# Kernel optimization log

Hardware: AMD Instinct MI355X
Metric: run time of the kernel (lower is better)

## Reference

```python
import jax, jax.numpy as jnp
import numpy as np

WS = 7           # window size
NH = 12          # num heads
EPS_ADA = 1e-6   # AdaLayerNorm eps
EPS_LN = 1e-5    # torch nn.LayerNorm default eps


def _rel_pos_index(ws):
    coords = np.stack(np.meshgrid(np.arange(ws), np.arange(ws), indexing='ij'))  # (2,ws,ws)
    flat = coords.reshape(2, -1)                      # (2, N)
    rel = flat[:, :, None] - flat[:, None, :]         # (2, N, N)
    rel = rel.transpose(1, 2, 0).astype(np.int64)     # (N, N, 2)
    rel[:, :, 0] += ws - 1
    rel[:, :, 1] += ws - 1
    rel[:, :, 0] *= 2 * ws - 1
    return jnp.asarray(rel.sum(-1))                   # (N, N) in [0, (2ws-1)^2)

REL_IDX = _rel_pos_index(WS)


def setup_inputs() -> dict:
    key = jax.random.key(0)
    ks = jax.random.split(key, 8)
    B, H, W, C, COND = 32, 56, 56, 384, 128
    L = H * W
    s = 0.02
    return {
        'x_tok': jax.random.normal(ks[0], (B, L, C), jnp.float32),
        'z_tok': jax.random.normal(ks[1], (B, L, C), jnp.float32),
        'cond': jax.random.normal(ks[2], (B, COND), jnp.float32),
        'gamma_x': jnp.ones((C,), jnp.float32),
        'beta_x': jnp.zeros((C,), jnp.float32),
        'mod_w': jax.random.normal(ks[3], (COND, 2 * C), jnp.float32) * s,
        'mod_b': jnp.zeros((2 * C,), jnp.float32),
        'gamma_z': jnp.ones((C,), jnp.float32),
        'beta_z': jnp.zeros((C,), jnp.float32),
        'rel_bias_table': jax.random.normal(ks[4], ((2 * WS - 1) ** 2, NH), jnp.float32) * s,
        'q_w': jax.random.normal(ks[5], (C, C), jnp.float32) * s,
        'q_b': jnp.zeros((C,), jnp.float32),
        'kv_w': jax.random.normal(ks[6], (C, 2 * C), jnp.float32) * s,
        'kv_b': jnp.zeros((2 * C,), jnp.float32),
        'proj_w': jax.random.normal(ks[7], (C, C), jnp.float32) * s,
        'proj_b': jnp.zeros((C,), jnp.float32),
        'H': H,
        'W': W,
    }


def reference(x_tok, z_tok, cond, gamma_x, beta_x, mod_w, mod_b,
              gamma_z, beta_z, rel_bias_table, q_w, q_b, kv_w, kv_b,
              proj_w, proj_b, H, W):
    B, L, C = x_tok.shape
    hd = C // NH
    N = WS * WS

    # AdaLayerNorm-Zero on x
    mu = x_tok.mean(-1, keepdims=True)
    var = ((x_tok - mu) ** 2).mean(-1, keepdims=True)
    x_hat = (x_tok - mu) * jax.lax.rsqrt(var + EPS_ADA)
    mod = (cond @ mod_w + mod_b).reshape(B, 2, C)
    d_gamma, d_beta = mod[:, 0], mod[:, 1]
    x = (gamma_x * (1.0 + d_gamma))[:, None, :] * x_hat + (beta_x + d_beta)[:, None, :]

    # LayerNorm on z
    mz = z_tok.mean(-1, keepdims=True)
    vz = ((z_tok - mz) ** 2).mean(-1, keepdims=True)
    z = (z_tok - mz) * jax.lax.rsqrt(vz + EPS_LN) * gamma_z + beta_z

    # window partition: (B,H,W,C) -> (B*nW, N, C)
    def part(t):
        t = t.reshape(B, H // WS, WS, W // WS, WS, C)
        return t.transpose(0, 1, 3, 2, 4, 5).reshape(-1, N, C)

    x_win = part(x.reshape(B, H, W, C))
    z_win = part(z.reshape(B, H, W, C))

    # cross window attention
    q = (x_win @ q_w + q_b).reshape(-1, N, NH, hd).transpose(0, 2, 1, 3)  # (Bw,H,N,d)
    kv = (z_win @ kv_w + kv_b).reshape(-1, N, 2, NH, hd)
    k = kv[:, :, 0].transpose(0, 2, 1, 3)
    v = kv[:, :, 1].transpose(0, 2, 1, 3)
    scale = hd ** -0.5
    attn = jnp.einsum('bhnd,bhmd->bhnm', q * scale, k)                    # (Bw,H,N,N)
    bias = rel_bias_table[REL_IDX.reshape(-1)].reshape(N, N, NH).transpose(2, 0, 1)
    attn = jax.nn.softmax(attn + bias[None], axis=-1)
    out = jnp.einsum('bhnm,bhmd->bhnd', attn, v).transpose(0, 2, 1, 3).reshape(-1, N, C)
    out = out @ proj_w + proj_b

    # window reverse: (B*nW, N, C) -> (B, L, C)
    fused = out.reshape(B, H // WS, W // WS, WS, WS, C)
    fused = fused.transpose(0, 1, 3, 2, 4, 5).reshape(B, L, C)

    return x_tok + fused
```

## Files before the change

### kernel.cpp

```cpp
#include <hip/hip_runtime.h>
#include <hip/hip_bf16.h>

typedef float f32x4 __attribute__((ext_vector_type(4)));
typedef short short8 __attribute__((ext_vector_type(8)));
typedef __hip_bfloat16 bf16;

constexpr int CDIM  = 384;
constexpr int LTOK  = 3136;
constexpr int NWIN  = 2048;
constexpr int MROWS = 100352;
constexpr int MPAD  = MROWS + 64;
constexpr int NP64  = 1568;

__device__ __forceinline__ void gload_lds16(const void* g, void* l) {
  __builtin_amdgcn_global_load_lds(
      (const __attribute__((address_space(1))) void*)g,
      (__attribute__((address_space(3))) void*)l, 16, 0, 0);
}

__device__ __forceinline__ void row_to_bl(int r, int& b, int& l) {
  int w = r / 49, n = r % 49;
  b = w >> 6;
  int wrem = w & 63;
  int wy = wrem >> 3, wx = wrem & 7;
  int ny = n / 7, nx = n % 7;
  l = (wy * 7 + ny) * 56 + wx * 7 + nx;
}


__global__ __launch_bounds__(256) void prep_all(
    const float* __restrict__ cond, const float* __restrict__ mw,
    const float* __restrict__ mb, float* __restrict__ mod,
    const float* __restrict__ qw, const float* __restrict__ kvw,
    const float* __restrict__ pw,
    bf16* __restrict__ wtq, bf16* __restrict__ wtkv, bf16* __restrict__ wtp,
    const float* __restrict__ tab, float* __restrict__ bT) {
  int bid = blockIdx.x, t = threadIdx.x;
  if (bid < 96) {
    int idx = bid * 256 + t;
    int b = idx / 768, j = idx % 768;
    float s = mb[j];
    const float* cr = cond + b * 128;
    #pragma unroll 4
    for (int k = 0; k < 128; k++) s += cr[k] * mw[(size_t)k * 768 + j];
    mod[idx] = s;
  } else if (bid < 2400) {
    int idx = (bid - 96) * 256 + t;
    const float* src; bf16* dst; int i, Wn;
    if (idx < 147456)      { i = idx;          src = qw;  dst = wtq;  Wn = 384; }
    else if (idx < 442368) { i = idx - 147456; src = kvw; dst = wtkv; Wn = 768; }
    else                   { i = idx - 442368; src = pw;  dst = wtp;  Wn = 384; }
    int j = i & 7, nc = (i >> 3) & 63, g = (i >> 9) & 3;
    int kt = (i >> 11) % 12, s = i / 24576;
    int k = kt * 32 + g * 8 + j, n = s * 64 + nc;
    dst[i] = __float2bfloat16(src[(size_t)k * Wn + n]);
  } else {
    int idx = (bid - 2400) * 256 + t;
    int h = idx >> 12, rem = idx & 4095, m = rem >> 6, c = rem & 63;
    float v;
    if (c >= 49)      v = -1e30f;
    else if (m >= 49) v = 0.f;
    else {
      int yq = m / 7, xq = m % 7, yk = c / 7, xk = c % 7;
      v = tab[((yq - yk + 6) * 13 + (xq - xk + 6)) * 12 + h];
    }
    bT[idx] = v;
  }
}


struct alignas(8) B4 { bf16 h[4]; };

__global__ __launch_bounds__(256) void ln_both(
    const float* __restrict__ x_tok, const float* __restrict__ gx,
    const float* __restrict__ bx, const float* __restrict__ modbuf,
    const float* __restrict__ z_tok, const float* __restrict__ gz,
    const float* __restrict__ bz,
    bf16* __restrict__ xO, bf16* __restrict__ zO) {
  int bid = blockIdx.x;
  bool isX = bid < 25088;
  const float* src   = isX ? x_tok : z_tok;
  const float* gamma = isX ? gx : gz;
  const float* beta  = isX ? bx : bz;
  const float* mod   = isX ? modbuf : nullptr;
  bf16* dst          = isX ? xO : zO;
  float eps          = isX ? 1e-6f : 1e-5f;
  int rb = (isX ? bid : bid - 25088) * 4;

  int wid = threadIdx.x >> 6, lane = threadIdx.x & 63;
  int r = rb + wid;
  int bb, ll; row_to_bl(r, bb, ll);
  const f32x4* x4 = (const f32x4*)(src + ((size_t)bb * LTOK + ll) * 384);
  f32x4 a = x4[lane];
  f32x4 b = {0.f, 0.f, 0.f, 0.f};
  if (lane < 32) b = x4[64 + lane];
  float s  = a[0] + a[1] + a[2] + a[3] + b[0] + b[1] + b[2] + b[3];
  float s2 = a[0]*a[0] + a[1]*a[1] + a[2]*a[2] + a[3]*a[3]
           + b[0]*b[0] + b[1]*b[1] + b[2]*b[2] + b[3]*b[3];
  #pragma unroll
  for (int d = 1; d < 64; d <<= 1) { s += __shfl_xor(s, d); s2 += __shfl_xor(s2, d); }
  float mu = s * (1.f / 384.f);
  float var = s2 * (1.f / 384.f) - mu * mu;
  float rstd = rsqrtf(var + eps);
  bf16* o = dst + (size_t)r * 384;
  const f32x4* g4 = (const f32x4*)gamma;
  const f32x4* be4 = (const f32x4*)beta;
  if (mod != nullptr) {
    const f32x4* mg4 = (const f32x4*)(mod + bb * 768);
    const f32x4* mb4 = (const f32x4*)(mod + bb * 768 + 384);
    {
      f32x4 gg = g4[lane], bb2 = be4[lane], mg = mg4[lane], mb = mb4[lane];
      B4 p;
      #pragma unroll
      for (int i = 0; i < 4; i++)
        p.h[i] = __float2bfloat16((gg[i] * (1.f + mg[i])) * ((a[i] - mu) * rstd) + bb2[i] + mb[i]);
      *((B4*)o + lane) = p;
    }
    if (lane < 32) {
      f32x4 gg = g4[64 + lane], bb2 = be4[64 + lane], mg = mg4[64 + lane], mb = mb4[64 + lane];
      B4 p;
      #pragma unroll
      for (int i = 0; i < 4; i++)
        p.h[i] = __float2bfloat16((gg[i] * (1.f + mg[i])) * ((b[i] - mu) * rstd) + bb2[i] + mb[i]);
      *((B4*)o + 64 + lane) = p;
    }
  } else {
    {
      f32x4 gg = g4[lane], bb2 = be4[lane];
      B4 p;
      #pragma unroll
      for (int i = 0; i < 4; i++)
        p.h[i] = __float2bfloat16((a[i] - mu) * rstd * gg[i] + bb2[i]);
      *((B4*)o + lane) = p;
    }
    if (lane < 32) {
      f32x4 gg = g4[64 + lane], bb2 = be4[64 + lane];
      B4 p;
      #pragma unroll
      for (int i = 0; i < 4; i++)
        p.h[i] = __float2bfloat16((b[i] - mu) * rstd * gg[i] + bb2[i]);
      *((B4*)o + 64 + lane) = p;
    }
  }
}


template<int MODE>
__global__ __launch_bounds__(256, 4) void gemm6(
    const bf16* __restrict__ A, const bf16* __restrict__ WTt,
    const float* __restrict__ bias, void* __restrict__ outp,
    const float* __restrict__ resid, float scale, int N, int NS, int BPS) {
  __shared__ __align__(16) bf16 wS[24576];
  const int t = threadIdx.x;
  const int wid = t >> 6, lane = t & 63;
  const int r16 = lane & 15, g = lane >> 4;
  const int s = blockIdx.x % NS, bi = blockIdx.x / NS;

  {
    const char* src = (const char*)WTt + (size_t)s * 49152;
    #pragma unroll
    for (int i = 0; i < 12; i++)
      gload_lds16(src + (i * 256 + t) * 16, (char*)wS + (i * 256 + t) * 16);
  }
  float bc[4];
  #pragma unroll
  for (int ni = 0; ni < 4; ni++) bc[ni] = bias[s * 64 + ni * 16 + r16];
  __syncthreads();

  for (int p = bi; p < NP64; p += BPS) {
    const int prow = p * 64 + wid * 16;

    short8 aF[12];
    #pragma unroll
    for (int kt = 0; kt < 12; kt++)
      aF[kt] = *(const short8*)(A + (size_t)(prow + r16) * 384 + kt * 32 + g * 8);

    f32x4 acc[4] = {};
    #pragma unroll
    for (int kt = 0; kt < 12; kt++) {
      #pragma unroll
      for (int ni = 0; ni < 4; ni++) {
        short8 wF = *(const short8*)((const char*)wS + (kt * 4 + g) * 1024 + (ni * 16 + r16) * 16);
        acc[ni] = __builtin_amdgcn_mfma_f32_16x16x32_bf16(aF[kt], wF, acc[ni], 0, 0, 0);
      }
    }

    if (MODE == 0) {
      bf16* O = (bf16*)outp;
      #pragma unroll
      for (int rr = 0; rr < 4; rr++) {
        size_t rbase = (size_t)(prow + g * 4 + rr) * N + s * 64;
        #pragma unroll
        for (int ni = 0; ni < 4; ni++)
          O[rbase + ni * 16 + r16] = __float2bfloat16((acc[ni][rr] + bc[ni]) * scale);
      }
    } else {
      float* O = (float*)outp;
      #pragma unroll
      for (int rr = 0; rr < 4; rr++) {
        int row = prow + g * 4 + rr;
        int bb, ll; row_to_bl(row, bb, ll);
        size_t base = ((size_t)bb * LTOK + ll) * 384 + s * 64;
        #pragma unroll
        for (int ni = 0; ni < 4; ni++)
          O[base + ni * 16 + r16] = resid[base + ni * 16 + r16] + acc[ni][rr] + bc[ni];
      }
    }
  }
}


__global__ __launch_bounds__(64) void attn_kernel(
    const bf16* __restrict__ q, const bf16* __restrict__ kv,
    const float* __restrict__ biasT, bf16* __restrict__ o) {
  __shared__ __align__(16) bf16 vt[32][72];
  __shared__ __align__(16) bf16 P[64][72];
  const int h = blockIdx.x, w = blockIdx.y;
  const int lane = threadIdx.x;
  const int r16 = lane & 15, g = lane >> 4;
  const size_t qbase = (size_t)w * 49 * 384 + h * 32;
  const size_t kvbase = (size_t)w * 49 * 768 + h * 32;

  for (int e = lane; e < 32 * 72; e += 64) ((bf16*)vt)[e] = __float2bfloat16(0.f);
  for (int e = lane; e < 49 * 32; e += 64) {
    int c = e >> 5, d = e & 31;
    vt[d][c] = kv[kvbase + (size_t)c * 768 + 384 + d];
  }

  short8 aq[4], bk[4];
  #pragma unroll
  for (int mi = 0; mi < 4; mi++)
    aq[mi] = *(const short8*)(q + qbase + (size_t)(mi * 16 + r16) * 384 + g * 8);
  #pragma unroll
  for (int ni = 0; ni < 4; ni++)
    bk[ni] = *(const short8*)(kv + kvbase + (size_t)(ni * 16 + r16) * 768 + g * 8);

  f32x4 zero = {0.f, 0.f, 0.f, 0.f};
  f32x4 S[4][4];
  #pragma unroll
  for (int mi = 0; mi < 4; mi++)
    #pragma unroll
    for (int ni = 0; ni < 4; ni++)
      S[mi][ni] = __builtin_amdgcn_mfma_f32_16x16x32_bf16(aq[mi], bk[ni], zero, 0, 0, 0);

  const float* bt = biasT + h * 4096;
  #pragma unroll
  for (int mi = 0; mi < 4; mi++) {
    #pragma unroll
    for (int r = 0; r < 4; r++) {
      int rowm = mi * 16 + g * 4 + r;
      float sv[4];
      #pragma unroll
      for (int ni = 0; ni < 4; ni++)
        sv[ni] = S[mi][ni][r] + bt[rowm * 64 + ni * 16 + r16];
      float mx = fmaxf(fmaxf(sv[0], sv[1]), fmaxf(sv[2], sv[3]));
      #pragma unroll
      for (int d = 1; d < 16; d <<= 1) mx = fmaxf(mx, __shfl_xor(mx, d));
      float sum = 0.f;
      #pragma unroll
      for (int ni = 0; ni < 4; ni++) { sv[ni] = __expf(sv[ni] - mx); sum += sv[ni]; }
      #pragma unroll
      for (int d = 1; d < 16; d <<= 1) sum += __shfl_xor(sum, d);
      float inv = __fdividef(1.f, sum);
      #pragma unroll
      for (int ni = 0; ni < 4; ni++)
        P[rowm][ni * 16 + r16] = __float2bfloat16(sv[ni] * inv);
    }
  }
  __syncthreads();

  f32x4 acc[4][2] = {};
  #pragma unroll
  for (int c0 = 0; c0 < 2; c0++) {
    short8 ap[4], bv[2];
    #pragma unroll
    for (int mi = 0; mi < 4; mi++)
      ap[mi] = *(const short8*)((const char*)&P[0][0] + (mi * 16 + r16) * 144 + c0 * 64 + g * 16);
    #pragma unroll
    for (int di = 0; di < 2; di++)
      bv[di] = *(const short8*)((const char*)&vt[0][0] + (di * 16 + r16) * 144 + c0 * 64 + g * 16);
    #pragma unroll
    for (int mi = 0; mi < 4; mi++)
      #pragma unroll
      for (int di = 0; di < 2; di++)
        acc[mi][di] = __builtin_amdgcn_mfma_f32_16x16x32_bf16(ap[mi], bv[di], acc[mi][di], 0, 0, 0);
  }

  #pragma unroll
  for (int mi = 0; mi < 4; mi++) {
    #pragma unroll
    for (int r = 0; r < 4; r++) {
      int m = mi * 16 + g * 4 + r;
      if (m < 49) {
        #pragma unroll
        for (int di = 0; di < 2; di++)
          o[(size_t)(w * 49 + m) * 384 + h * 32 + di * 16 + r16] =
              __float2bfloat16(acc[mi][di][r]);
      }
    }
  }
}


extern "C" void kernel_launch(void* const* d_in, const int* in_sizes, int n_in,
                              void* d_out, int out_size, void* d_ws, size_t ws_size,
                              hipStream_t stream) {
  (void)in_sizes; (void)n_in; (void)out_size; (void)ws_size;
  const float* x_tok   = (const float*)d_in[0];
  const float* z_tok   = (const float*)d_in[1];
  const float* cond    = (const float*)d_in[2];
  const float* gamma_x = (const float*)d_in[3];
  const float* beta_x  = (const float*)d_in[4];
  const float* mod_w   = (const float*)d_in[5];
  const float* mod_b   = (const float*)d_in[6];
  const float* gamma_z = (const float*)d_in[7];
  const float* beta_z  = (const float*)d_in[8];
  const float* rel_tab = (const float*)d_in[9];
  const float* q_w     = (const float*)d_in[10];
  const float* q_b     = (const float*)d_in[11];
  const float* kv_w    = (const float*)d_in[12];
  const float* kv_b    = (const float*)d_in[13];
  const float* proj_w  = (const float*)d_in[14];
  const float* proj_b  = (const float*)d_in[15];

  char* ws = (char*)d_ws;
  float* modbuf = (float*)(ws + 0);
  bf16*  wtq    = (bf16*)(ws + 98304);
  bf16*  wtkv   = (bf16*)(ws + 98304 + 294912);
  bf16*  wtp    = (bf16*)(ws + 98304 + 294912 + 589824);
  float* biasT  = (float*)(ws + 98304 + 294912 + 589824 + 294912);
  char*  R1     = ws + 1474560;
  char*  R2     = R1 + (size_t)MPAD * 384 * 2;
  char*  R3     = R2 + (size_t)MPAD * 384 * 2;
  char*  R4     = R3 + (size_t)MPAD * 768 * 2;

  hipMemsetAsync(R2 + (size_t)MROWS * 384 * 2, 0, 64 * 384 * 2, stream);
  hipMemsetAsync(R3 + (size_t)MROWS * 768 * 2, 0, 64 * 768 * 2, stream);

  prep_all<<<2592, 256, 0, stream>>>(cond, mod_w, mod_b, modbuf,
                                     q_w, kv_w, proj_w, wtq, wtkv, wtp,
                                     rel_tab, biasT);
  ln_both<<<50176, 256, 0, stream>>>(x_tok, gamma_x, beta_x, modbuf,
                                     z_tok, gamma_z, beta_z,
                                     (bf16*)R1, (bf16*)R4);
  gemm6<0><<<768, 256, 0, stream>>>(
      (const bf16*)R1, wtq, q_b, R2, nullptr, 0.17677669529663687f, 384, 6, 128);
  gemm6<0><<<768, 256, 0, stream>>>(
      (const bf16*)R4, wtkv, kv_b, R3, nullptr, 1.0f, 768, 12, 64);
  attn_kernel<<<dim3(12, NWIN), 64, 0, stream>>>(
      (const bf16*)R2, (const bf16*)R3, biasT, (bf16*)R1);
  gemm6<1><<<768, 256, 0, stream>>>(
      (const bf16*)R1, wtp, proj_b, d_out, x_tok, 1.0f, 384, 6, 128);
}
```

Baseline: 704.6 us.

## Retile projection GEMMs to 128x32 blocks with 2x2 MFMA per wave

Each GEMM block now keeps a 32-column weight slice in LDS instead of 64 columns, halving shared memory and raising the occupancy target to 6 blocks per CU. Each wave computes a 32x32 tile (2x2 MFMA) rather than 16x64, and A fragments are loaded per k-step instead of being prefetched into 12 registers. The weight pre-layout is changed to match, and the grid is doubled with an x-swizzle so that groups of 8 blocks share row chunks. The intent is higher occupancy and better L2 locality for the A operand. In exchange, each A row tile is now read by twice as many column-slice blocks.

Measured after the change: 1.177 ms. 67.0% more time.

```diff
diff --git a/kernel.cpp b/kernel.cpp
--- a/kernel.cpp
+++ b/kernel.cpp
@@ -10,7 +10,7 @@
 constexpr int NWIN  = 2048;
 constexpr int MROWS = 100352;
 constexpr int MPAD  = MROWS + 64;
-constexpr int NP64  = 1568;
+constexpr int NP128 = 784;
 
 __device__ __forceinline__ void gload_lds16(const void* g, void* l) {
   __builtin_amdgcn_global_load_lds(
@@ -50,9 +50,11 @@
     if (idx < 147456)      { i = idx;          src = qw;  dst = wtq;  Wn = 384; }
     else if (idx < 442368) { i = idx - 147456; src = kvw; dst = wtkv; Wn = 768; }
     else                   { i = idx - 442368; src = pw;  dst = wtp;  Wn = 384; }
-    int j = i & 7, nc = (i >> 3) & 63, g = (i >> 9) & 3;
-    int kt = (i >> 11) % 12, s = i / 24576;
-    int k = kt * 32 + g * 8 + j, n = s * 64 + nc;
+    int s = i / 12288, rem = i % 12288;
+    int u = rem >> 8, v = rem & 255;
+    int ni = v >> 7, r16 = (v >> 3) & 15, j8 = v & 7;
+    int kt = u >> 2, g = u & 3;
+    int k = kt * 32 + g * 8 + j8, n = s * 32 + ni * 16 + r16;
     dst[i] = __float2bfloat16(src[(size_t)k * Wn + n]);
   } else {
     int idx = (bid - 2400) * 256 + t;
@@ -146,64 +148,68 @@
 
 
 template<int MODE>
-__global__ __launch_bounds__(256, 4) void gemm6(
+__global__ __launch_bounds__(256, 6) void gemm7(
     const bf16* __restrict__ A, const bf16* __restrict__ WTt,
     const float* __restrict__ bias, void* __restrict__ outp,
-    const float* __restrict__ resid, float scale, int N, int NS, int BPS) {
-  __shared__ __align__(16) bf16 wS[24576];
+    const float* __restrict__ resid, float scale, int N, int NS, int NC) {
+  __shared__ __align__(16) bf16 wS[12288];
   const int t = threadIdx.x;
   const int wid = t >> 6, lane = t & 63;
   const int r16 = lane & 15, g = lane >> 4;
-  const int s = blockIdx.x % NS, bi = blockIdx.x / NS;
+  const int x = blockIdx.x & 7, i = blockIdx.x >> 3;
+  const int s = i % NS;
+  const int c = (i / NS) * 8 + x;
 
   {
-    const char* src = (const char*)WTt + (size_t)s * 49152;
-    #pragma unroll
-    for (int i = 0; i < 12; i++)
-      gload_lds16(src + (i * 256 + t) * 16, (char*)wS + (i * 256 + t) * 16);
-  }
-  float bc[4];
-  #pragma unroll
-  for (int ni = 0; ni < 4; ni++) bc[ni] = bias[s * 64 + ni * 16 + r16];
+    const char* src = (const char*)WTt + (size_t)s * 24576;
+    #pragma unroll
+    for (int k = 0; k < 6; k++)
+      gload_lds16(src + (k * 256 + t) * 16, (char*)wS + (k * 256 + t) * 16);
+  }
+  const float bc0 = bias[s * 32 + r16];
+  const float bc1 = bias[s * 32 + 16 + r16];
   __syncthreads();
 
-  for (int p = bi; p < NP64; p += BPS) {
-    const int prow = p * 64 + wid * 16;
-
-    short8 aF[12];
-    #pragma unroll
-    for (int kt = 0; kt < 12; kt++)
-      aF[kt] = *(const short8*)(A + (size_t)(prow + r16) * 384 + kt * 32 + g * 8);
-
-    f32x4 acc[4] = {};
+  for (int p = c; p < NP128; p += NC) {
+    const int prow = p * 128 + wid * 32;
+    const bf16* Ab = A + (size_t)prow * 384;
+
+    f32x4 acc[2][2] = {};
     #pragma unroll
     for (int kt = 0; kt < 12; kt++) {
-      #pragma unroll
-      for (int ni = 0; ni < 4; ni++) {
-        short8 wF = *(const short8*)((const char*)wS + (kt * 4 + g) * 1024 + (ni * 16 + r16) * 16);
-        acc[ni] = __builtin_amdgcn_mfma_f32_16x16x32_bf16(aF[kt], wF, acc[ni], 0, 0, 0);
-      }
+      short8 a0 = *(const short8*)(Ab + (size_t)r16 * 384 + kt * 32 + g * 8);
+      short8 a1 = *(const short8*)(Ab + (size_t)(16 + r16) * 384 + kt * 32 + g * 8);
+      short8 w0 = *(const short8*)((const char*)wS + (kt * 4 + g) * 512 + r16 * 16);
+      short8 w1 = *(const short8*)((const char*)wS + (kt * 4 + g) * 512 + 256 + r16 * 16);
+      acc[0][0] = __builtin_amdgcn_mfma_f32_16x16x32_bf16(a0, w0, acc[0][0], 0, 0, 0);
+      acc[0][1] = __builtin_amdgcn_mfma_f32_16x16x32_bf16(a0, w1, acc[0][1], 0, 0, 0);
+      acc[1][0] = __builtin_amdgcn_mfma_f32_16x16x32_bf16(a1, w0, acc[1][0], 0, 0, 0);
+      acc[1][1] = __builtin_amdgcn_mfma_f32_16x16x32_bf16(a1, w1, acc[1][1], 0, 0, 0);
     }
 
     if (MODE == 0) {
       bf16* O = (bf16*)outp;
       #pragma unroll
-      for (int rr = 0; rr < 4; rr++) {
-        size_t rbase = (size_t)(prow + g * 4 + rr) * N + s * 64;
+      for (int m = 0; m < 2; m++) {
         #pragma unroll
-        for (int ni = 0; ni < 4; ni++)
-          O[rbase + ni * 16 + r16] = __float2bfloat16((acc[ni][rr] + bc[ni]) * scale);
+        for (int rr = 0; rr < 4; rr++) {
+          size_t rbase = (size_t)(prow + m * 16 + g * 4 + rr) * N + s * 32;
+          O[rbase + r16]      = __float2bfloat16((acc[m][0][rr] + bc0) * scale);
+          O[rbase + 16 + r16] = __float2bfloat16((acc[m][1][rr] + bc1) * scale);
+        }
       }
     } else {
       float* O = (float*)outp;
       #pragma unroll
-      for (int rr = 0; rr < 4; rr++) {
-        int row = prow + g * 4 + rr;
-        int bb, ll; row_to_bl(row, bb, ll);
-        size_t base = ((size_t)bb * LTOK + ll) * 384 + s * 64;
+      for (int m = 0; m < 2; m++) {
         #pragma unroll
-        for (int ni = 0; ni < 4; ni++)
-          O[base + ni * 16 + r16] = resid[base + ni * 16 + r16] + acc[ni][rr] + bc[ni];
+        for (int rr = 0; rr < 4; rr++) {
+          int row = prow + m * 16 + g * 4 + rr;
+          int bb, ll; row_to_bl(row, bb, ll);
+          size_t base = ((size_t)bb * LTOK + ll) * 384 + s * 32;
+          O[base + r16]      = resid[base + r16]      + acc[m][0][rr] + bc0;
+          O[base + 16 + r16] = resid[base + 16 + r16] + acc[m][1][rr] + bc1;
+        }
       }
     }
   }
@@ -343,12 +349,12 @@
   ln_both<<<50176, 256, 0, stream>>>(x_tok, gamma_x, beta_x, modbuf,
                                      z_tok, gamma_z, beta_z,
                                      (bf16*)R1, (bf16*)R4);
-  gemm6<0><<<768, 256, 0, stream>>>(
-      (const bf16*)R1, wtq, q_b, R2, nullptr, 0.17677669529663687f, 384, 6, 128);
-  gemm6<0><<<768, 256, 0, stream>>>(
-      (const bf16*)R4, wtkv, kv_b, R3, nullptr, 1.0f, 768, 12, 64);
+  gemm7<0><<<1536, 256, 0, stream>>>(
+      (const bf16*)R1, wtq, q_b, R2, nullptr, 0.17677669529663687f, 384, 12, 128);
+  gemm7<0><<<1536, 256, 0, stream>>>(
+      (const bf16*)R4, wtkv, kv_b, R3, nullptr, 1.0f, 768, 24, 64);
   attn_kernel<<<dim3(12, NWIN), 64, 0, stream>>>(
       (const bf16*)R2, (const bf16*)R3, biasT, (bf16*)R1);
-  gemm6<1><<<768, 256, 0, stream>>>(
-      (const bf16*)R1, wtp, proj_b, d_out, x_tok, 1.0f, 384, 6, 128);
-}
+  gemm7<1><<<1536, 256, 0, stream>>>(
+      (const bf16*)R1, wtp, proj_b, d_out, x_tok, 1.0f, 384, 12, 128);
+}
```

## Fuse Q/KV projection, window attention and output projection into one per-window kernel

Applied to the files above, without the earlier changes.

Replaces the three GEMM launches and the separate attention kernel with a single kernel per window. Each block stages the window's normalized x and z rows in swizzled LDS, and each wavefront computes Q, K and V for three heads, runs softmax attention, and writes the result back into LDS. The block then applies the output projection with the residual add. This removes the global round trips for Q, KV and the attention output, and the padding memsets. In exchange it uses about 153KB of LDS per block (one block per CU), reads weight fragments straight from global/L2 on every window instead of holding them in LDS, and pads the 49 rows to 64.

Result: slower. 806.3 us (+14.4%).

```diff
diff --git a/kernel.cpp b/kernel.cpp
--- a/kernel.cpp
+++ b/kernel.cpp
@@ -5,18 +5,11 @@
 typedef short short8 __attribute__((ext_vector_type(8)));
 typedef __hip_bfloat16 bf16;
 
-constexpr int CDIM  = 384;
 constexpr int LTOK  = 3136;
 constexpr int NWIN  = 2048;
 constexpr int MROWS = 100352;
-constexpr int MPAD  = MROWS + 64;
-constexpr int NP64  = 1568;
-
-__device__ __forceinline__ void gload_lds16(const void* g, void* l) {
-  __builtin_amdgcn_global_load_lds(
-      (const __attribute__((address_space(1))) void*)g,
-      (__attribute__((address_space(3))) void*)l, 16, 0, 0);
-}
+
+#define MFMA(a, b, c) __builtin_amdgcn_mfma_f32_16x16x32_bf16((a), (b), (c), 0, 0, 0)
 
 __device__ __forceinline__ void row_to_bl(int r, int& b, int& l) {
   int w = r / 49, n = r % 49;
@@ -50,9 +43,11 @@
     if (idx < 147456)      { i = idx;          src = qw;  dst = wtq;  Wn = 384; }
     else if (idx < 442368) { i = idx - 147456; src = kvw; dst = wtkv; Wn = 768; }
     else                   { i = idx - 442368; src = pw;  dst = wtp;  Wn = 384; }
-    int j = i & 7, nc = (i >> 3) & 63, g = (i >> 9) & 3;
-    int kt = (i >> 11) % 12, s = i / 24576;
-    int k = kt * 32 + g * 8 + j, n = s * 64 + nc;
+    int s = i / 12288, rem = i % 12288;
+    int u = rem >> 8, v = rem & 255;
+    int ni = v >> 7, r16 = (v >> 3) & 15, j8 = v & 7;
+    int kt = u >> 2, g = u & 3;
+    int k = kt * 32 + g * 8 + j8, n = s * 32 + ni * 16 + r16;
     dst[i] = __float2bfloat16(src[(size_t)k * Wn + n]);
   } else {
     int idx = (bid - 2400) * 256 + t;
@@ -145,158 +140,217 @@
 }
 
 
-template<int MODE>
-__global__ __launch_bounds__(256, 4) void gemm6(
-    const bf16* __restrict__ A, const bf16* __restrict__ WTt,
-    const float* __restrict__ bias, void* __restrict__ outp,
-    const float* __restrict__ resid, float scale, int N, int NS, int BPS) {
-  __shared__ __align__(16) bf16 wS[24576];
-  const int t = threadIdx.x;
-  const int wid = t >> 6, lane = t & 63;
-  const int r16 = lane & 15, g = lane >> 4;
-  const int s = blockIdx.x % NS, bi = blockIdx.x / NS;
-
-  {
-    const char* src = (const char*)WTt + (size_t)s * 49152;
-    #pragma unroll
-    for (int i = 0; i < 12; i++)
-      gload_lds16(src + (i * 256 + t) * 16, (char*)wS + (i * 256 + t) * 16);
-  }
-  float bc[4];
+__global__ __launch_bounds__(256, 1) void fused_win(
+    const bf16* __restrict__ xh, const bf16* __restrict__ zh,
+    const bf16* __restrict__ wtq, const bf16* __restrict__ wtkv,
+    const bf16* __restrict__ wtp,
+    const float* __restrict__ qb, const float* __restrict__ kvb,
+    const float* __restrict__ pb, const float* __restrict__ biasT,
+    const float* __restrict__ resid, float* __restrict__ out) {
+  __shared__ __align__(16) char L[157184];
+  const int t = threadIdx.x, w = blockIdx.x;
+  const int wid = t >> 6, lane = t & 63, r16 = lane & 15, g = lane >> 4;
+  const f32x4 zero = {0.f, 0.f, 0.f, 0.f};
+
+  for (int slot = t; slot < 4704; slot += 256) {
+    int s = slot / 2352, rem = slot % 2352;
+    int row = rem / 48, c8 = rem % 48;
+    const bf16* src = (s ? zh : xh) + (size_t)(w * 49 + row) * 384 + c8 * 8;
+    short8 v = *(const short8*)src;
+    *(short8*)(L + s * 37632 + row * 768 + ((c8 * 16) ^ ((row & 7) << 4))) = v;
+  }
+  __syncthreads();
+
+  const int hw = (wid + w) & 3;
+  char* qS = L + 75264 + wid * 20480;
+  char* kS = qS + 4096;
+  char* vS = qS + 8192;
+  char* pS = qS + 12288;
+
+  f32x4 pv[3][4][2] = {};
+
   #pragma unroll
-  for (int ni = 0; ni < 4; ni++) bc[ni] = bias[s * 64 + ni * 16 + r16];
+  for (int i = 0; i < 3; i++) {
+    const int h = hw * 3 + i;
+
+    f32x4 qa[4][2] = {};
+    #pragma unroll
+    for (int kt = 0; kt < 12; kt++) {
+      short8 xf[4];
+      #pragma unroll
+      for (int m = 0; m < 3; m++) {
+        int row = m * 16 + r16;
+        xf[m] = *(const short8*)(L + row * 768 + ((kt * 64 + g * 16) ^ ((row & 7) << 4)));
+      }
+      xf[3] = *(const short8*)(L + 48 * 768 + kt * 64 + g * 16);
+      const short8* wq = (const short8*)(wtq + (size_t)h * 12288 + (kt * 4 + g) * 256 + r16 * 8);
+      short8 w0 = wq[0], w1 = wq[16];
+      #pragma unroll
+      for (int m = 0; m < 4; m++) {
+        qa[m][0] = MFMA(xf[m], w0, qa[m][0]);
+        qa[m][1] = MFMA(xf[m], w1, qa[m][1]);
+      }
+    }
+    #pragma unroll
+    for (int ni = 0; ni < 2; ni++) {
+      float bc = qb[h * 32 + ni * 16 + r16];
+      #pragma unroll
+      for (int m = 0; m < 4; m++)
+        #pragma unroll
+        for (int rr = 0; rr < 4; rr++) {
+          int row = m * 16 + g * 4 + rr;
+          *(bf16*)(qS + row * 64 + (ni * 16 + r16) * 2) =
+              __float2bfloat16((qa[m][ni][rr] + bc) * 0.17677669529663687f);
+        }
+    }
+
+    f32x4 ka[4][2] = {}, va[4][2] = {};
+    #pragma unroll
+    for (int kt = 0; kt < 12; kt++) {
+      short8 zf[4];
+      #pragma unroll
+      for (int m = 0; m < 3; m++) {
+        int row = m * 16 + r16;
+        zf[m] = *(const short8*)(L + 37632 + row * 768 + ((kt * 64 + g * 16) ^ ((row & 7) << 4)));
+      }
+      zf[3] = *(const short8*)(L + 37632 + 48 * 768 + kt * 64 + g * 16);
+      const short8* wk = (const short8*)(wtkv + (size_t)h * 12288 + (kt * 4 + g) * 256 + r16 * 8);
+      const short8* wv = (const short8*)(wtkv + (size_t)(12 + h) * 12288 + (kt * 4 + g) * 256 + r16 * 8);
+      short8 k0 = wk[0], k1 = wk[16], v0 = wv[0], v1 = wv[16];
+      #pragma unroll
+      for (int m = 0; m < 4; m++) {
+        ka[m][0] = MFMA(zf[m], k0, ka[m][0]);
+        ka[m][1] = MFMA(zf[m], k1, ka[m][1]);
+        va[m][0] = MFMA(zf[m], v0, va[m][0]);
+        va[m][1] = MFMA(zf[m], v1, va[m][1]);
+      }
+    }
+    #pragma unroll
+    for (int ni = 0; ni < 2; ni++) {
+      float bck = kvb[h * 32 + ni * 16 + r16];
+      float bcv = kvb[384 + h * 32 + ni * 16 + r16];
+      #pragma unroll
+      for (int m = 0; m < 4; m++) {
+        B4 pk;
+        #pragma unroll
+        for (int rr = 0; rr < 4; rr++) {
+          int row = m * 16 + g * 4 + rr;
+          *(bf16*)(kS + row * 64 + (ni * 16 + r16) * 2) = __float2bfloat16(ka[m][ni][rr] + bck);
+          pk.h[rr] = __float2bfloat16(va[m][ni][rr] + bcv);
+        }
+        *(B4*)(vS + (ni * 16 + r16) * 128 + (m * 16 + g * 4) * 2) = pk;
+      }
+    }
+
+    short8 aq[4], bk[4];
+    #pragma unroll
+    for (int m = 0; m < 4; m++) aq[m] = *(const short8*)(qS + (m * 16 + r16) * 64 + g * 16);
+    #pragma unroll
+    for (int n = 0; n < 4; n++) bk[n] = *(const short8*)(kS + (n * 16 + r16) * 64 + g * 16);
+    f32x4 S[4][4];
+    #pragma unroll
+    for (int m = 0; m < 4; m++)
+      #pragma unroll
+      for (int n = 0; n < 4; n++)
+        S[m][n] = MFMA(aq[m], bk[n], zero);
+
+    const float* bt = biasT + h * 4096;
+    #pragma unroll
+    for (int m = 0; m < 4; m++) {
+      #pragma unroll
+      for (int rr = 0; rr < 4; rr++) {
+        int rowm = m * 16 + g * 4 + rr;
+        float sv[4];
+        #pragma unroll
+        for (int n = 0; n < 4; n++)
+          sv[n] = S[m][n][rr] + bt[rowm * 64 + n * 16 + r16];
+        float mx = fmaxf(fmaxf(sv[0], sv[1]), fmaxf(sv[2], sv[3]));
+        #pragma unroll
+        for (int d = 1; d < 16; d <<= 1) mx = fmaxf(mx, __shfl_xor(mx, d));
+        float sum = 0.f;
+        #pragma unroll
+        for (int n = 0; n < 4; n++) { sv[n] = __expf(sv[n] - mx); sum += sv[n]; }
+        #pragma unroll
+        for (int d = 1; d < 16; d <<= 1) sum += __shfl_xor(sum, d);
+        float inv = __fdividef(1.f, sum);
+        #pragma unroll
+        for (int n = 0; n < 4; n++)
+          *(bf16*)(pS + rowm * 128 + (n * 16 + r16) * 2) = __float2bfloat16(sv[n] * inv);
+      }
+    }
+
+    #pragma unroll
+    for (int c0 = 0; c0 < 2; c0++) {
+      short8 pa[4], bv[2];
+      #pragma unroll
+      for (int m = 0; m < 4; m++)
+        pa[m] = *(const short8*)(pS + (m * 16 + r16) * 128 + c0 * 64 + g * 16);
+      #pragma unroll
+      for (int d = 0; d < 2; d++)
+        bv[d] = *(const short8*)(vS + (d * 16 + r16) * 128 + c0 * 64 + g * 16);
+      #pragma unroll
+      for (int m = 0; m < 4; m++)
+        #pragma unroll
+        for (int d = 0; d < 2; d++)
+          pv[i][m][d] = MFMA(pa[m], bv[d], pv[i][m][d]);
+    }
+  }
+
   __syncthreads();
-
-  for (int p = bi; p < NP64; p += BPS) {
-    const int prow = p * 64 + wid * 16;
-
-    short8 aF[12];
-    #pragma unroll
-    for (int kt = 0; kt < 12; kt++)
-      aF[kt] = *(const short8*)(A + (size_t)(prow + r16) * 384 + kt * 32 + g * 8);
-
-    f32x4 acc[4] = {};
+  #pragma unroll
+  for (int i = 0; i < 3; i++) {
+    int h = hw * 3 + i;
+    #pragma unroll
+    for (int d = 0; d < 2; d++) {
+      int col = h * 32 + d * 16 + r16;
+      #pragma unroll
+      for (int m = 0; m < 4; m++)
+        #pragma unroll
+        for (int rr = 0; rr < 4; rr++) {
+          int row = m * 16 + g * 4 + rr;
+          if (row < 49)
+            *(bf16*)(L + row * 768 + ((col * 2) ^ ((row & 7) << 4))) =
+                __float2bfloat16(pv[i][m][d][rr]);
+        }
+    }
+  }
+  __syncthreads();
+
+  #pragma unroll
+  for (int si = 0; si < 3; si++) {
+    int sl = hw * 3 + si;
+    f32x4 ac[4][2] = {};
     #pragma unroll
     for (int kt = 0; kt < 12; kt++) {
-      #pragma unroll
-      for (int ni = 0; ni < 4; ni++) {
-        short8 wF = *(const short8*)((const char*)wS + (kt * 4 + g) * 1024 + (ni * 16 + r16) * 16);
-        acc[ni] = __builtin_amdgcn_mfma_f32_16x16x32_bf16(aF[kt], wF, acc[ni], 0, 0, 0);
-      }
-    }
-
-    if (MODE == 0) {
-      bf16* O = (bf16*)outp;
-      #pragma unroll
-      for (int rr = 0; rr < 4; rr++) {
-        size_t rbase = (size_t)(prow + g * 4 + rr) * N + s * 64;
-        #pragma unroll
-        for (int ni = 0; ni < 4; ni++)
-          O[rbase + ni * 16 + r16] = __float2bfloat16((acc[ni][rr] + bc[ni]) * scale);
-      }
-    } else {
-      float* O = (float*)outp;
-      #pragma unroll
-      for (int rr = 0; rr < 4; rr++) {
-        int row = prow + g * 4 + rr;
-        int bb, ll; row_to_bl(row, bb, ll);
-        size_t base = ((size_t)bb * LTOK + ll) * 384 + s * 64;
-        #pragma unroll
-        for (int ni = 0; ni < 4; ni++)
-          O[base + ni * 16 + r16] = resid[base + ni * 16 + r16] + acc[ni][rr] + bc[ni];
-      }
-    }
-  }
-}
-
-
-__global__ __launch_bounds__(64) void attn_kernel(
-    const bf16* __restrict__ q, const bf16* __restrict__ kv,
-    const float* __restrict__ biasT, bf16* __restrict__ o) {
-  __shared__ __align__(16) bf16 vt[32][72];
-  __shared__ __align__(16) bf16 P[64][72];
-  const int h = blockIdx.x, w = blockIdx.y;
-  const int lane = threadIdx.x;
-  const int r16 = lane & 15, g = lane >> 4;
-  const size_t qbase = (size_t)w * 49 * 384 + h * 32;
-  const size_t kvbase = (size_t)w * 49 * 768 + h * 32;
-
-  for (int e = lane; e < 32 * 72; e += 64) ((bf16*)vt)[e] = __float2bfloat16(0.f);
-  for (int e = lane; e < 49 * 32; e += 64) {
-    int c = e >> 5, d = e & 31;
-    vt[d][c] = kv[kvbase + (size_t)c * 768 + 384 + d];
-  }
-
-  short8 aq[4], bk[4];
-  #pragma unroll
-  for (int mi = 0; mi < 4; mi++)
-    aq[mi] = *(const short8*)(q + qbase + (size_t)(mi * 16 + r16) * 384 + g * 8);
-  #pragma unroll
-  for (int ni = 0; ni < 4; ni++)
-    bk[ni] = *(const short8*)(kv + kvbase + (size_t)(ni * 16 + r16) * 768 + g * 8);
-
-  f32x4 zero = {0.f, 0.f, 0.f, 0.f};
-  f32x4 S[4][4];
-  #pragma unroll
-  for (int mi = 0; mi < 4; mi++)
-    #pragma unroll
-    for (int ni = 0; ni < 4; ni++)
-      S[mi][ni] = __builtin_amdgcn_mfma_f32_16x16x32_bf16(aq[mi], bk[ni], zero, 0, 0, 0);
-
-  const float* bt = biasT + h * 4096;
-  #pragma unroll
-  for (int mi = 0; mi < 4; mi++) {
-    #pragma unroll
-    for (int r = 0; r < 4; r++) {
-      int rowm = mi * 16 + g * 4 + r;
-      float sv[4];
-      #pragma unroll
-      for (int ni = 0; ni < 4; ni++)
-        sv[ni] = S[mi][ni][r] + bt[rowm * 64 + ni * 16 + r16];
-      float mx = fmaxf(fmaxf(sv[0], sv[1]), fmaxf(sv[2], sv[3]));
-      #pragma unroll
-      for (int d = 1; d < 16; d <<= 1) mx = fmaxf(mx, __shfl_xor(mx, d));
-      float sum = 0.f;
-      #pragma unroll
-      for (int ni = 0; ni < 4; ni++) { sv[ni] = __expf(sv[ni] - mx); sum += sv[ni]; }
-      #pragma unroll
-      for (int d = 1; d < 16; d <<= 1) sum += __shfl_xor(sum, d);
-      float inv = __fdividef(1.f, sum);
-      #pragma unroll
-      for (int ni = 0; ni < 4; ni++)
-        P[rowm][ni * 16 + r16] = __float2bfloat16(sv[ni] * inv);
-    }
-  }
-  __syncthreads();
-
-  f32x4 acc[4][2] = {};
-  #pragma unroll
-  for (int c0 = 0; c0 < 2; c0++) {
-    short8 ap[4], bv[2];
-    #pragma unroll
-    for (int mi = 0; mi < 4; mi++)
-      ap[mi] = *(const short8*)((const char*)&P[0][0] + (mi * 16 + r16) * 144 + c0 * 64 + g * 16);
-    #pragma unroll
-    for (int di = 0; di < 2; di++)
-      bv[di] = *(const short8*)((const char*)&vt[0][0] + (di * 16 + r16) * 144 + c0 * 64 + g * 16);
-    #pragma unroll
-    for (int mi = 0; mi < 4; mi++)
-      #pragma unroll
-      for (int di = 0; di < 2; di++)
-        acc[mi][di] = __builtin_amdgcn_mfma_f32_16x16x32_bf16(ap[mi], bv[di], acc[mi][di], 0, 0, 0);
-  }
-
-  #pragma unroll
-  for (int mi = 0; mi < 4; mi++) {
-    #pragma unroll
-    for (int r = 0; r < 4; r++) {
-      int m = mi * 16 + g * 4 + r;
-      if (m < 49) {
-        #pragma unroll
-        for (int di = 0; di < 2; di++)
-          o[(size_t)(w * 49 + m) * 384 + h * 32 + di * 16 + r16] =
-              __float2bfloat16(acc[mi][di][r]);
-      }
+      short8 af[4];
+      #pragma unroll
+      for (int m = 0; m < 4; m++) {
+        int row = m * 16 + r16;
+        af[m] = *(const short8*)(L + row * 768 + ((kt * 64 + g * 16) ^ ((row & 7) << 4)));
+      }
+      const short8* wp = (const short8*)(wtp + (size_t)sl * 12288 + (kt * 4 + g) * 256 + r16 * 8);
+      short8 p0 = wp[0], p1 = wp[16];
+      #pragma unroll
+      for (int m = 0; m < 4; m++) {
+        ac[m][0] = MFMA(af[m], p0, ac[m][0]);
+        ac[m][1] = MFMA(af[m], p1, ac[m][1]);
+      }
+    }
+    #pragma unroll
+    for (int ni = 0; ni < 2; ni++) {
+      int col = sl * 32 + ni * 16 + r16;
+      float bc = pb[col];
+      #pragma unroll
+      for (int m = 0; m < 4; m++)
+        #pragma unroll
+        for (int rr = 0; rr < 4; rr++) {
+          int row = m * 16 + g * 4 + rr;
+          if (row < 49) {
+            int bb, ll; row_to_bl(w * 49 + row, bb, ll);
+            size_t base = ((size_t)bb * LTOK + ll) * 384;
+            out[base + col] = resid[base + col] + ac[m][ni][rr] + bc;
+          }
+        }
     }
   }
 }
@@ -329,26 +383,15 @@
   bf16*  wtkv   = (bf16*)(ws + 98304 + 294912);
   bf16*  wtp    = (bf16*)(ws + 98304 + 294912 + 589824);
   float* biasT  = (float*)(ws + 98304 + 294912 + 589824 + 294912);
-  char*  R1     = ws + 1474560;
-  char*  R2     = R1 + (size_t)MPAD * 384 * 2;
-  char*  R3     = R2 + (size_t)MPAD * 384 * 2;
-  char*  R4     = R3 + (size_t)MPAD * 768 * 2;
-
-  hipMemsetAsync(R2 + (size_t)MROWS * 384 * 2, 0, 64 * 384 * 2, stream);
-  hipMemsetAsync(R3 + (size_t)MROWS * 768 * 2, 0, 64 * 768 * 2, stream);
+  bf16*  R1     = (bf16*)(ws + 1474560);
+  bf16*  R4     = R1 + (size_t)MROWS * 384;
 
   prep_all<<<2592, 256, 0, stream>>>(cond, mod_w, mod_b, modbuf,
                                      q_w, kv_w, proj_w, wtq, wtkv, wtp,
                                      rel_tab, biasT);
   ln_both<<<50176, 256, 0, stream>>>(x_tok, gamma_x, beta_x, modbuf,
-                                     z_tok, gamma_z, beta_z,
-                                     (bf16*)R1, (bf16*)R4);
-  gemm6<0><<<768, 256, 0, stream>>>(
-      (const bf16*)R1, wtq, q_b, R2, nullptr, 0.17677669529663687f, 384, 6, 128);
-  gemm6<0><<<768, 256, 0, stream>>>(
-      (const bf16*)R4, wtkv, kv_b, R3, nullptr, 1.0f, 768, 12, 64);
-  attn_kernel<<<dim3(12, NWIN), 64, 0, stream>>>(
-      (const bf16*)R2, (const bf16*)R3, biasT, (bf16*)R1);
-  gemm6<1><<<768, 256, 0, stream>>>(
-      (const bf16*)R1, wtp, proj_b, d_out, x_tok, 1.0f, 384, 6, 128);
-}
+                                     z_tok, gamma_z, beta_z, R1, R4);
+  fused_win<<<NWIN, 256, 0, stream>>>(R1, R4, wtq, wtkv, wtp,
+                                      q_b, kv_b, proj_b, biasT,
+                                      x_tok, (float*)d_out);
+}
```
